# Kernel tuning notes

Measured on AMD Instinct MI355X. Metric: run time of the kernel, lower is better.

## Reference

```python
import jax, jax.numpy as jnp
import numpy as np

HEAD_SIZE = 64
N_EMBED = 1024

def setup_inputs() -> dict:
    key = jax.random.key(0)
    kx, kk, kq, kv = jax.random.split(key, 4)
    x = jax.random.normal(kx, (8, 2048, N_EMBED), dtype=jnp.float32)
    # torch nn.Linear weights: [out_features, in_features]
    s = 1.0 / np.sqrt(N_EMBED)
    Wk = jax.random.uniform(kk, (HEAD_SIZE, N_EMBED), jnp.float32, -s, s)
    Wq = jax.random.uniform(kq, (HEAD_SIZE, N_EMBED), jnp.float32, -s, s)
    Wv = jax.random.uniform(kv, (HEAD_SIZE, N_EMBED), jnp.float32, -s, s)
    return {"x": x, "Wk": Wk, "Wq": Wq, "Wv": Wv}

def reference(x, Wk, Wq, Wv):
    B, T, C = x.shape
    k = x @ Wk.T  # [B,T,H]
    q = x @ Wq.T
    v = x @ Wv.T
    # NOTE: original computes k @ q^T and scales by sqrt(C)=sqrt(n_embed)
    wei = jnp.einsum('btd,bsd->bts', k, q) / jnp.sqrt(jnp.float32(C))
    mask = jnp.tril(jnp.ones((T, T), dtype=bool))
    wei = jnp.where(mask, wei, -jnp.inf)
    wei = jax.nn.softmax(wei, axis=-1)
    return wei @ v  # [B,T,H]
```

## Files before the change

kernel.cpp:

```cpp
#include <hip/hip_runtime.h>
#include <hip/hip_bf16.h>


typedef __attribute__((ext_vector_type(8))) short short8;
typedef __attribute__((ext_vector_type(4))) float f32x4;
typedef __attribute__((ext_vector_type(16))) float f32x16;
typedef unsigned int u32;

#define BATCH 8
#define T 2048
#define CDIM 1024
#define HD 64
#define QK_SCALE 0.04508422f

static __device__ __forceinline__ short f2bf(float f) {
    return __builtin_bit_cast(short, __float2bfloat16(f));
}
static __device__ __forceinline__ float bf2f(unsigned short s) {
    u32 u = ((u32)s) << 16;
    return __builtin_bit_cast(float, u);
}
static __device__ __forceinline__ u32 packbf(float lo, float hi) {
    return (u32)(unsigned short)f2bf(lo) | ((u32)(unsigned short)f2bf(hi) << 16);
}
static __device__ __forceinline__ f32x4 mfma16(short8 a, short8 b, f32x4 c) {
    return __builtin_amdgcn_mfma_f32_16x16x32_bf16(a, b, c, 0, 0, 0);
}
static __device__ __forceinline__ f32x16 mfma32(short8 a, short8 b, f32x16 c) {
    return __builtin_amdgcn_mfma_f32_32x32x16_bf16(a, b, c, 0, 0, 0);
}

#define SOFT_BARRIER { \
    __builtin_amdgcn_sched_barrier(0); \
    asm volatile("s_waitcnt lgkmcnt(0)" ::: "memory"); \
    __builtin_amdgcn_s_barrier(); \
    __builtin_amdgcn_sched_barrier(0); }

__global__ __launch_bounds__(256) void wcvt_kernel(
    const float* __restrict__ Wk, const float* __restrict__ Wq,
    const float* __restrict__ Wv, short* __restrict__ wfrag)
{
    const int t = blockIdx.x * 256 + threadIdx.x;
    const int lane = t & 63, kk = (t >> 6) & 31, d16 = (t >> 11) & 3, p = t >> 13;
    const float* __restrict__ W = (p == 0) ? Wk : (p == 1 ? Wq : Wv);
    const float sc = (p == 0) ? QK_SCALE : 1.0f;
    const float* src = W + (size_t)(d16 * 16 + (lane & 15)) * CDIM
                         + kk * 32 + ((lane >> 4) & 3) * 8;
    f32x4 a = *(const f32x4*)src;
    f32x4 b = *(const f32x4*)(src + 4);
    short8 o;
#pragma unroll
    for (int e = 0; e < 4; ++e) { o[e] = f2bf(a[e] * sc); o[e + 4] = f2bf(b[e] * sc); }
    *(short8*)(wfrag + (size_t)t * 8) = o;
}

#define XLOAD(KC) { \
    xr0 = *(const f32x4*)(xsrc + (KC) * 64); \
    xr1 = *(const f32x4*)(xsrc + (KC) * 64 + 4); }

#define XWRITE(BASE) { \
    short8 v = { f2bf(xr0[0]), f2bf(xr0[1]), f2bf(xr0[2]), f2bf(xr0[3]), \
                 f2bf(xr1[0]), f2bf(xr1[1]), f2bf(xr1[2]), f2bf(xr1[3]) }; \
    *(short8*)((BASE) + srow * 128 + ((sseg * 16) ^ ((srow & 7) << 4))) = v; }

#define BLOAD(DST, KC) \
    _Pragma("unroll") for (int u = 0; u < 6; ++u) \
        DST[u] = *(const short8*)&wfrag[(size_t)((cg * 3 + (u % 3)) * 32 + (KC) * 2 + (u / 3)) * 512 + lane * 8];

#define COMPUTE(XBASE, B) \
    _Pragma("unroll") for (int kkL = 0; kkL < 2; ++kkL) { \
        short8 af0 = *(short8*)((XBASE) + c * 128 + ((kkL * 64 + g * 16) ^ ((c & 7) << 4))); \
        short8 af1 = *(short8*)((XBASE) + (16 + c) * 128 + ((kkL * 64 + g * 16) ^ ((c & 7) << 4))); \
        _Pragma("unroll") for (int j = 0; j < 3; ++j) { \
            acc[0][j] = mfma16(af0, B[kkL * 3 + j], acc[0][j]); \
            acc[1][j] = mfma16(af1, B[kkL * 3 + j], acc[1][j]); } }

__global__ __launch_bounds__(256) void proj_kernel(
    const float* __restrict__ x, const short* __restrict__ wfrag,
    short* __restrict__ kfrag, short* __restrict__ qfrag, short* __restrict__ vfrag)
{
    __shared__ __align__(16) char lds[16384];
    char* X0 = lds;
    char* X1 = lds + 4096;

    const int tid = threadIdx.x, cg = tid >> 6, lane = tid & 63;
    const int c = lane & 15, g = lane >> 4;
    const int srow = tid >> 3, sseg = tid & 7;
    const int row0 = blockIdx.x * 32;
    const float* __restrict__ xsrc = x + (size_t)(row0 + srow) * CDIM + sseg * 8;

    f32x4 acc[2][3] = {};
    short8 bA[6], bB[6];
    f32x4 xr0, xr1;

    XLOAD(0)
    XWRITE(X0)
    BLOAD(bA, 0)
    SOFT_BARRIER

    for (int c2 = 0; c2 < 8; ++c2) {
        const int cB = 2 * c2 + 1;
        BLOAD(bB, cB)
        XLOAD(cB)
        COMPUTE(X0, bA)
        XWRITE(X1)
        SOFT_BARRIER
        if (c2 < 7) {
            BLOAD(bA, cB + 1)
            XLOAD(cB + 1)
        }
        COMPUTE(X1, bB)
        if (c2 < 7) {
            XWRITE(X0)
        }
        SOFT_BARRIER
    }

    short* st_k = (short*)lds;
    short* st_q = (short*)(lds + 4608);
    short* st_v = (short*)(lds + 9216);
#pragma unroll
    for (int j = 0; j < 3; ++j) {
        const int q = cg * 3 + j, p = q >> 2, d16 = q & 3;
#pragma unroll
        for (int rh = 0; rh < 2; ++rh)
#pragma unroll
            for (int r = 0; r < 4; ++r) {
                const int mrow = rh * 16 + g * 4 + r;
                const short v = f2bf(acc[rh][j][r]);
                if (p == 0)      st_k[mrow * 72 + d16 * 16 + c] = v;
                else if (p == 1) st_q[mrow * 72 + d16 * 16 + c] = v;
                else             st_v[(d16 * 16 + c) * 40 + mrow] = v;
            }
    }
    __syncthreads();

    const int b = row0 >> 11, i = (row0 & 2047) >> 5;
    const size_t tb = ((size_t)(b * 64 + i)) * 4;
    const int l5 = lane & 31, h = lane >> 5;
    const int fq = cg;

    short8 kv = *(short8*)&st_k[l5 * 72 + fq * 16 + h * 8];
    *(short8*)&kfrag[(tb + fq) * 512 + lane * 8] = kv;
    short8 qv = *(short8*)&st_q[l5 * 72 + fq * 16 + h * 8];
    *(short8*)&qfrag[(tb + fq) * 512 + lane * 8] = qv;
    const int dh = fq >> 1, ssub = fq & 1;
    short8 vv = *(short8*)&st_v[(dh * 32 + l5) * 40 + ssub * 16 + h * 8];
    *(short8*)&vfrag[(tb + fq) * 512 + lane * 8] = vv;
}

__global__ __launch_bounds__(512) void attn_kernel(
    const short* __restrict__ kfrag, const short* __restrict__ qfrag,
    const short* __restrict__ vfrag, float* __restrict__ out)
{
    const int tid = threadIdx.x, wid = tid >> 6, lane = tid & 63;
    const int l5 = lane & 31, h = lane >> 5;
    const int bx = blockIdx.x;
    const int i = 63 - (bx >> 3);
    const int b = bx & 7;
    const int t0 = i * 32;

    __shared__ u32   sO[8][32][32];
    __shared__ float sML[8][2][32];

    const short* __restrict__ kb = kfrag + ((size_t)(b * 64 + i)) * 2048;
    const short* __restrict__ qb = qfrag + ((size_t)b * 64) * 2048;
    const short* __restrict__ vb = vfrag + ((size_t)b * 64) * 2048;

    short8 kf[4];
#pragma unroll
    for (int ks = 0; ks < 4; ++ks)
        kf[ks] = *(const short8*)&kb[ks * 512 + lane * 8];

    float m = -1e30f, l = 0.f;
    f32x16 o0 = {}, o1 = {};

    short8 qf[4], vf[4], qn[4], vn[4];
#pragma unroll
    for (int ks = 0; ks < 4; ++ks) {
        qf[ks] = *(const short8*)&qb[((size_t)wid * 4 + ks) * 512 + lane * 8];
        vf[ks] = *(const short8*)&vb[((size_t)wid * 4 + ks) * 512 + lane * 8];
    }

    for (int st = wid; st <= i; st += 8) {
        f32x16 Cs = {};
#pragma unroll
        for (int ks = 0; ks < 4; ++ks)
            Cs = mfma32(qf[ks], kf[ks], Cs);

        if (st + 8 <= i) {
#pragma unroll
            for (int ks = 0; ks < 4; ++ks) {
                qn[ks] = *(const short8*)&qb[((size_t)(st + 8) * 4 + ks) * 512 + lane * 8];
                vn[ks] = *(const short8*)&vb[((size_t)(st + 8) * 4 + ks) * 512 + lane * 8];
            }
        }

        if (st == i) {
#pragma unroll
            for (int r = 0; r < 16; ++r) {
                const int srow = (r & 3) + 8 * (r >> 2) + 4 * h;
                if (srow > l5) Cs[r] = -1e30f;
            }
        }
        float mx = fmaxf(Cs[0], Cs[1]);
#pragma unroll
        for (int r = 2; r < 16; ++r) mx = fmaxf(mx, Cs[r]);
        mx = fmaxf(mx, __shfl_xor(mx, 32));
        if (!__all(mx <= m)) {
            const float mnew = fmaxf(m, mx);
            const float alpha = exp2f(m - mnew);
            m = mnew;
            l *= alpha;
#pragma unroll
            for (int r = 0; r < 16; ++r) { o0[r] *= alpha; o1[r] *= alpha; }
        }
        u32 pk[8];
        float rs = 0.f;
#pragma unroll
        for (int q = 0; q < 8; ++q) {
            const float e0 = exp2f(Cs[2 * q] - m);
            const float e1 = exp2f(Cs[2 * q + 1] - m);
            rs += e0 + e1;
            pk[q] = packbf(e0, e1);
        }
        rs += __shfl_xor(rs, 32);
        l += rs;

        u32 w0 = pk[0], w2 = pk[2];
        asm volatile("v_permlane32_swap_b32 %0, %1" : "+v"(w0), "+v"(w2));
        u32 w1 = pk[1], w3 = pk[3];
        asm volatile("v_permlane32_swap_b32 %0, %1" : "+v"(w1), "+v"(w3));
        u32 w4 = pk[4], w6 = pk[6];
        asm volatile("v_permlane32_swap_b32 %0, %1" : "+v"(w4), "+v"(w6));
        u32 w5 = pk[5], w7 = pk[7];
        asm volatile("v_permlane32_swap_b32 %0, %1" : "+v"(w5), "+v"(w7));
        short8 pf0, pf1;
        pf0[0] = (short)(w0 & 0xffff); pf0[1] = (short)(w0 >> 16);
        pf0[2] = (short)(w1 & 0xffff); pf0[3] = (short)(w1 >> 16);
        pf0[4] = (short)(w2 & 0xffff); pf0[5] = (short)(w2 >> 16);
        pf0[6] = (short)(w3 & 0xffff); pf0[7] = (short)(w3 >> 16);
        pf1[0] = (short)(w4 & 0xffff); pf1[1] = (short)(w4 >> 16);
        pf1[2] = (short)(w5 & 0xffff); pf1[3] = (short)(w5 >> 16);
        pf1[4] = (short)(w6 & 0xffff); pf1[5] = (short)(w6 >> 16);
        pf1[6] = (short)(w7 & 0xffff); pf1[7] = (short)(w7 >> 16);

        o0 = mfma32(vf[0], pf0, o0);
        o0 = mfma32(vf[1], pf1, o0);
        o1 = mfma32(vf[2], pf0, o1);
        o1 = mfma32(vf[3], pf1, o1);

#pragma unroll
        for (int ks = 0; ks < 4; ++ks) { qf[ks] = qn[ks]; vf[ks] = vn[ks]; }
    }

#pragma unroll
    for (int q = 0; q < 8; ++q) {
        const int dp = (q & 1) + 4 * (q >> 1) + 2 * h;
        sO[wid][dp][l5]      = packbf(o0[2 * q], o0[2 * q + 1]);
        sO[wid][16 + dp][l5] = packbf(o1[2 * q], o1[2 * q + 1]);
    }
    if (h == 0) { sML[wid][0][l5] = m; sML[wid][1][l5] = l; }
    __syncthreads();

    float M = -1e30f;
#pragma unroll
    for (int p = 0; p < 8; ++p) M = fmaxf(M, sML[p][0][l5]);
    float L = 0.f;
    float av[4] = {};
#pragma unroll
    for (int p = 0; p < 8; ++p) {
        const float w = exp2f(sML[p][0][l5] - M);
        L += w * sML[p][1][l5];
#pragma unroll
        for (int dd2 = 0; dd2 < 2; ++dd2) {
            const u32 v = sO[p][wid * 4 + h * 2 + dd2][l5];
            av[2 * dd2]     += w * bf2f((unsigned short)(v & 0xffff));
            av[2 * dd2 + 1] += w * bf2f((unsigned short)(v >> 16));
        }
    }
    const float inv = 1.f / L;
    f32x4 r = { av[0] * inv, av[1] * inv, av[2] * inv, av[3] * inv };
    *(f32x4*)&out[((size_t)b * T + t0 + l5) * HD + wid * 8 + h * 4] = r;
}

extern "C" void kernel_launch(void* const* d_in, const int* in_sizes, int n_in,
                              void* d_out, int out_size, void* d_ws, size_t ws_size,
                              hipStream_t stream) {
    const float* x  = (const float*)d_in[0];
    const float* Wk = (const float*)d_in[1];
    const float* Wq = (const float*)d_in[2];
    const float* Wv = (const float*)d_in[3];
    float* out = (float*)d_out;

    short* kfrag = (short*)d_ws;
    short* qfrag = kfrag + (size_t)BATCH * T * HD;
    short* vfrag = qfrag + (size_t)BATCH * T * HD;
    short* wfrag = vfrag + (size_t)BATCH * T * HD;

    wcvt_kernel<<<96, 256, 0, stream>>>(Wk, Wq, Wv, wfrag);
    proj_kernel<<<512, 256, 0, stream>>>(x, wfrag, kfrag, qfrag, vfrag);
    attn_kernel<<<512, 512, 0, stream>>>(kfrag, qfrag, vfrag, out);
}
```

Measured before the change: 43.62 us.

## Triple-buffer LDS x tiles in projection kernel with deeper prefetch

Restructures the projection GEMM main loop from a 2-way ping-pong into a fully unrolled 16-step loop with three rotating LDS buffers. Global x loads now run two chunks ahead and weight fragments one chunk ahead. The write of the next tile goes to a buffer no wave is reading, so each step needs only one barrier instead of two. The cost is more LDS (12KB of the 16KB), more live registers for in-flight loads and fragments, and a larger unrolled code body.

```diff
diff --git a/kernel.cpp b/kernel.cpp
--- a/kernel.cpp
+++ b/kernel.cpp
@@ -80,8 +80,6 @@
     short* __restrict__ kfrag, short* __restrict__ qfrag, short* __restrict__ vfrag)
 {
     __shared__ __align__(16) char lds[16384];
-    char* X0 = lds;
-    char* X1 = lds + 4096;
 
     const int tid = threadIdx.x, cg = tid >> 6, lane = tid & 63;
     const int c = lane & 15, g = lane >> 4;
@@ -90,30 +88,28 @@
     const float* __restrict__ xsrc = x + (size_t)(row0 + srow) * CDIM + sseg * 8;
 
     f32x4 acc[2][3] = {};
-    short8 bA[6], bB[6];
+    short8 bC[6], bN[6];
     f32x4 xr0, xr1;
 
     XLOAD(0)
-    XWRITE(X0)
-    BLOAD(bA, 0)
-    SOFT_BARRIER
-
-    for (int c2 = 0; c2 < 8; ++c2) {
-        const int cB = 2 * c2 + 1;
-        BLOAD(bB, cB)
-        XLOAD(cB)
-        COMPUTE(X0, bA)
-        XWRITE(X1)
+    XWRITE(lds)
+    XLOAD(1)
+    BLOAD(bC, 0)
+    __syncthreads();
+
+#pragma unroll
+    for (int k = 0; k < 16; ++k) {
+        char* pc = lds + (k % 3) * 4096;
+        char* pw = lds + ((k + 1) % 3) * 4096;
+        if (k < 15) { XWRITE(pw) }
+        if (k < 14) { XLOAD(k + 2) }
+        if (k < 15) { BLOAD(bN, k + 1) }
+        COMPUTE(pc, bC)
         SOFT_BARRIER
-        if (c2 < 7) {
-            BLOAD(bA, cB + 1)
-            XLOAD(cB + 1)
-        }
-        COMPUTE(X1, bB)
-        if (c2 < 7) {
-            XWRITE(X0)
-        }
-        SOFT_BARRIER
+        if (k < 15) {
+#pragma unroll
+            for (int u = 0; u < 6; ++u) bC[u] = bN[u];
+        }
     }
 
     short* st_k = (short*)lds;
```

Result: no change. 43.63 us (+0.0%).
